# Kernel optimization log

Hardware: AMD Instinct MI355X
Metric: run time of the kernel (lower is better)

Reference implementation:

```python
import jax, jax.numpy as jnp
import numpy as np

CIN = 28
HID1, HID2 = 64, 64
U_IDX, V_IDX = 11, 12
MU_U, SD_U = 0.02, 0.15
MU_V, SD_V = -0.01, 0.12


def setup_inputs() -> dict:
    key = jax.random.key(0)
    ks = jax.random.split(key, 18)
    B, T, H, W = 8, 8, 128, 128
    s = 0.05
    f32 = jnp.float32
    d = {
        "x": jax.random.normal(ks[0], (B, T, CIN, H, W), f32),
        # reduce: Conv2d(Cin, 24, 1)
        "W_red": jax.random.normal(ks[1], (24, CIN), f32) * s,
        "b_red": jnp.zeros((24,), f32),
        # l1: LSTMCell(24, HID1) + Conv2d(HID1, HID1, 1)
        "Wih1": jax.random.normal(ks[2], (4 * HID1, 24), f32) * s,
        "Whh1": jax.random.normal(ks[3], (4 * HID1, HID1), f32) * s,
        "bih1": jnp.zeros((4 * HID1,), f32),
        "bhh1": jnp.zeros((4 * HID1,), f32),
        "Wc1": jax.random.normal(ks[4], (HID1, HID1), f32) * s,
        "bc1": jnp.zeros((HID1,), f32),
        # l2: LSTMCell(HID1, HID2) + Conv2d(HID2, HID2, 1)
        "Wih2": jax.random.normal(ks[5], (4 * HID2, HID1), f32) * s,
        "Whh2": jax.random.normal(ks[6], (4 * HID2, HID2), f32) * s,
        "bih2": jnp.zeros((4 * HID2,), f32),
        "bhh2": jnp.zeros((4 * HID2,), f32),
        "Wc2": jax.random.normal(ks[7], (HID2, HID2), f32) * s,
        "bc2": jnp.zeros((HID2,), f32),
        # head: Conv2d(HID2, 1, 1)
        "W_head": jax.random.normal(ks[8], (1, HID2), f32) * s,
        "b_head": jnp.zeros((1,), f32),
    }
    return d


def _lstm_cell(flat, h, c, Wih, Whh, bih, bhh):
    # PyTorch LSTMCell gate order: i, f, g, o
    g = flat @ Wih.T + bih + h @ Whh.T + bhh
    i, f, gg, o = jnp.split(g, 4, axis=1)
    c = jax.nn.sigmoid(f) * c + jax.nn.sigmoid(i) * jnp.tanh(gg)
    h = jax.nn.sigmoid(o) * jnp.tanh(c)
    return h, c


def _conv1x1(x, W, b):
    # x: [B,C,H,W], W: [O,C]
    return jnp.einsum('bchw,oc->bohw', x, W) + b[None, :, None, None]


def reference(x, W_red, b_red, Wih1, Whh1, bih1, bhh1, Wc1, bc1,
              Wih2, Whh2, bih2, bhh2, Wc2, bc2, W_head, b_head):
    B, T, C, H, W = x.shape
    N = B * H * W
    # de-normalize u/v channels for every timestep (dropout p=0 -> identity)
    x = x.at[:, :, U_IDX].set(x[:, :, U_IDX] * SD_U + MU_U)
    x = x.at[:, :, V_IDX].set(x[:, :, V_IDX] * SD_V + MU_V)

    def step(carry, frame):
        h1, c1, h2, c2 = carry
        inp = _conv1x1(frame, W_red, b_red)                 # [B,24,H,W]
        flat1 = inp.transpose(0, 2, 3, 1).reshape(N, 24)    # pixel-wise rows
        h1, c1 = _lstm_cell(flat1, h1, c1, Wih1, Whh1, bih1, bhh1)
        h1_map = h1.reshape(B, H, W, HID1).transpose(0, 3, 1, 2)
        o1 = _conv1x1(h1_map, Wc1, bc1)                     # [B,HID1,H,W]
        flat2 = o1.transpose(0, 2, 3, 1).reshape(N, HID1)
        h2, c2 = _lstm_cell(flat2, h2, c2, Wih2, Whh2, bih2, bhh2)
        return (h1, c1, h2, c2), None

    z1 = jnp.zeros((N, HID1), x.dtype)
    z2 = jnp.zeros((N, HID2), x.dtype)
    xs = jnp.transpose(x, (1, 0, 2, 3, 4))                  # [T,B,C,H,W]
    (h1, c1, h2, c2), _ = jax.lax.scan(step, (z1, z1, z2, z2), xs)
    # only the last o2 is used by the head
    h2_map = h2.reshape(B, H, W, HID2).transpose(0, 3, 1, 2)
    o2 = _conv1x1(h2_map, Wc2, bc2)                         # [B,HID2,H,W]
    out = _conv1x1(o2, W_head, b_head)                      # [B,1,H,W]
    return out[:, 0]                                        # squeeze(1) -> [B,H,W]
```

## Files before the change

### kernel.cpp

```cpp
#include <hip/hip_runtime.h>

typedef _Float16 f16;
typedef _Float16 f16x4 __attribute__((ext_vector_type(4)));
typedef _Float16 f16x8 __attribute__((ext_vector_type(8)));
typedef float f32x4 __attribute__((ext_vector_type(4)));

#define CIN 28
#define TT 8
#define HW 16384

#define S_SIG  (-1.44269504088896341f)
#define S_TANH ( 2.88539008177792681f)

#define WS_WX    0
#define WS_WHH1  16384
#define WS_W21   49152
#define WS_WHH2  81920
#define WS_BX    114688
#define WS_B2    115712
#define WS_WH    116736
#define WS_BH    116992

__device__ __forceinline__ float lstm_act(float gi, float gf, float gg, float go,
                                          float& c) {
  const float Ei = __builtin_amdgcn_exp2f(gi);
  const float Ef = __builtin_amdgcn_exp2f(gf);
  const float Eg = __builtin_amdgcn_exp2f(gg);
  const float Eo = __builtin_amdgcn_exp2f(go);
  const float pig = (1.f + Ei) * (1.f + Eg);
  const float pf  = 1.f + Ef;
  const float r3  = __builtin_amdgcn_rcpf(pig * pf);
  const float t1  = (Eg - 1.f) * pf;
  const float cn  = r3 * __builtin_fmaf(pig, c, t1);
  c = cn;
  const float Ec  = __builtin_amdgcn_exp2f(cn * S_TANH);
  const float roc = __builtin_amdgcn_rcpf((1.f + Eo) * (1.f + Ec));
  return (Ec - 1.f) * roc;
}

__global__ __launch_bounds__(64) void prep_kernel(
    const float* __restrict__ W_red, const float* __restrict__ b_red,
    const float* __restrict__ Wih1, const float* __restrict__ Whh1,
    const float* __restrict__ bih1, const float* __restrict__ bhh1,
    const float* __restrict__ Wc1,  const float* __restrict__ bc1,
    const float* __restrict__ Wih2, const float* __restrict__ Whh2,
    const float* __restrict__ bih2, const float* __restrict__ bhh2,
    const float* __restrict__ Wc2,  const float* __restrict__ bc2,
    const float* __restrict__ W_head, const float* __restrict__ b_head,
    unsigned char* __restrict__ ws)
{
  const int g = blockIdx.x;
  const int k = threadIdx.x;
  f16* WxH   = (f16*)(ws + WS_WX);
  f16* Whh1H = (f16*)(ws + WS_WHH1);
  f16* W21H  = (f16*)(ws + WS_W21);
  f16* Whh2H = (f16*)(ws + WS_WHH2);
  float* BX  = (float*)(ws + WS_BX);
  float* B2  = (float*)(ws + WS_B2);
  float* WHp = (float*)(ws + WS_WH);
  float* BHp = (float*)(ws + WS_BH);

  const float sc = ((g >> 6) == 2) ? S_TANH : S_SIG;

  float wxv = 0.f;
  if (k < CIN) {
    float s = 0.f;
    for (int r = 0; r < 24; ++r) s += Wih1[g*24 + r] * W_red[r*28 + k];
    wxv = s;
  }
  const float wx11 = __shfl(wxv, 11, 64);
  const float wx12 = __shfl(wxv, 12, 64);
  if (k == 11) wxv *= 0.15f;
  if (k == 12) wxv *= 0.12f;
  if (k < 32) WxH[g*32 + k] = (f16)(wxv * sc);

  Whh1H[g*64 + k] = (f16)(Whh1[g*64 + k] * sc);
  Whh2H[g*64 + k] = (f16)(Whh2[g*64 + k] * sc);

  {
    float s = 0.f;
    for (int m = 0; m < 64; ++m) s += Wih2[g*64 + m] * Wc1[m*64 + k];
    W21H[g*64 + k] = (f16)(s * sc);
  }

  if (k == 0) {
    float bx = bih1[g] + bhh1[g];
    for (int r = 0; r < 24; ++r) bx += Wih1[g*24 + r] * b_red[r];
    bx += wx11 * 0.02f + wx12 * (-0.01f);
    BX[g] = bx * sc;
    float b2v = bih2[g] + bhh2[g];
    for (int m = 0; m < 64; ++m) b2v += Wih2[g*64 + m] * bc1[m];
    B2[g] = b2v * sc;
  }
  if (g == 0) {
    float s = 0.f;
    for (int m = 0; m < 64; ++m) s += W_head[m] * Wc2[m*64 + k];
    WHp[k] = s;
    if (k == 0) {
      float s2 = b_head[0];
      for (int m = 0; m < 64; ++m) s2 += W_head[m] * bc2[m];
      BHp[0] = s2;
    }
  }
}

__global__ __launch_bounds__(256)
__attribute__((amdgpu_waves_per_eu(2, 2)))
void convlstm_main(
    const float* __restrict__ x, const unsigned char* __restrict__ ws,
    float* __restrict__ out)
{
  __shared__ __align__(16) f16 xs[2][64 * 40];
  __shared__ __align__(16) f16 h1buf[2][64 * 72];
  __shared__ __align__(16) f16 h2buf[2][64 * 72];

  const int tid  = threadIdx.x;
  const int lane = tid & 63;
  const int wv   = tid >> 6;
  const int cl   = lane & 15;
  const int qd   = lane >> 4;

  const f16* WxG   = (const f16*)(ws + WS_WX);
  const f16* Whh1G = (const f16*)(ws + WS_WHH1);
  const f16* W21G  = (const f16*)(ws + WS_W21);
  const f16* Whh2G = (const f16*)(ws + WS_WHH2);
  const float* BX  = (const float*)(ws + WS_BX);
  const float* B2  = (const float*)(ws + WS_B2);

  f16x8 wx[4];
  f16x8 whh1k0[4], whh1k1[4];
  f16x8 w21k0[4],  w21k1[4];
  f16x8 whh2k0[4], whh2k1[4];
  f32x4 bxq[4], b2q[4];
#pragma unroll
  for (int P = 0; P < 4; ++P) {
    const int gr = 64*P + 16*wv + cl;
    wx[P]     = *(const f16x8*)(WxG + gr*32 + qd*8);
    whh1k0[P] = *(const f16x8*)(Whh1G + gr*64 + qd*8);
    whh1k1[P] = *(const f16x8*)(Whh1G + gr*64 + 32 + qd*8);
    w21k0[P]  = *(const f16x8*)(W21G  + gr*64 + qd*8);
    w21k1[P]  = *(const f16x8*)(W21G  + gr*64 + 32 + qd*8);
    whh2k0[P] = *(const f16x8*)(Whh2G + gr*64 + qd*8);
    whh2k1[P] = *(const f16x8*)(Whh2G + gr*64 + 32 + qd*8);
    bxq[P] = *(const f32x4*)(BX + 64*P + 16*wv + 4*qd);
    b2q[P] = *(const f32x4*)(B2 + 64*P + 16*wv + 4*qd);
  }

  {
    unsigned* z1 = (unsigned*)&h1buf[0][0];
    unsigned* z2 = (unsigned*)&h2buf[0][0];
#pragma unroll
    for (int i = tid; i < 2304; i += 256) { z1[i] = 0u; z2[i] = 0u; }
  }

  const int gpix = blockIdx.x * 64;
  const float* xb = x + (size_t)(gpix >> 14) * (TT * CIN * HW) + (gpix & (HW - 1));

  const int sp = lane;
  const int cb = wv * 8;

  {
    f16x8 v;
#pragma unroll
    for (int j = 0; j < 8; ++j) {
      const int ch = cb + j;
      v[j] = (ch < CIN) ? (f16)xb[ch*HW + sp] : (f16)0.f;
    }
    *(f16x8*)(&xs[0][sp*40 + cb]) = v;
  }
  __syncthreads();

  float c1s[4][4];
  float c2s[4][4];
#pragma unroll
  for (int a = 0; a < 4; ++a)
#pragma unroll
    for (int b = 0; b < 4; ++b) { c1s[a][b] = 0.f; c2s[a][b] = 0.f; }

#pragma unroll 1
  for (int t = 0; t < TT; ++t) {
    f16x8 xrv;
    if (t + 1 < TT) {
      const float* xt = xb + (size_t)(t + 1) * (CIN * HW);
#pragma unroll
      for (int j = 0; j < 8; ++j) {
        const int ch = cb + j;
        xrv[j] = (ch < CIN) ? (f16)xt[ch*HW + sp] : (f16)0.f;
      }
    }

    const f16* xsr = xs[t & 1];
    const f16* h1r = h1buf[t & 1];
    const f16* h2r = h2buf[t & 1];
    f16* h1w = h1buf[(t + 1) & 1];
    f16* h2w = h2buf[(t + 1) & 1];

#pragma unroll
    for (int mb = 0; mb < 4; ++mb) {
      const int p = 16*mb + cl;
      const f16x8 ax  = *(const f16x8*)(xsr + p*40 + qd*8);
      const f16x8 ah0 = *(const f16x8*)(h1r + p*72 + qd*8);
      const f16x8 ah1 = *(const f16x8*)(h1r + p*72 + 32 + qd*8);
      f32x4 acc[4];
#pragma unroll
      for (int P = 0; P < 4; ++P) {
        acc[P] = __builtin_amdgcn_mfma_f32_16x16x32_f16(whh1k0[P], ah0, bxq[P], 0, 0, 0);
        acc[P] = __builtin_amdgcn_mfma_f32_16x16x32_f16(whh1k1[P], ah1, acc[P], 0, 0, 0);
        acc[P] = __builtin_amdgcn_mfma_f32_16x16x32_f16(wx[P],     ax,  acc[P], 0, 0, 0);
      }
      float hn[4];
#pragma unroll
      for (int r = 0; r < 4; ++r)
        hn[r] = lstm_act(acc[0][r], acc[1][r], acc[2][r], acc[3][r], c1s[mb][r]);
      f16x4 hv; hv[0] = (f16)hn[0]; hv[1] = (f16)hn[1];
      hv[2] = (f16)hn[2]; hv[3] = (f16)hn[3];
      *(f16x4*)(h1w + p*72 + 16*wv + 4*qd) = hv;
    }
    __syncthreads();

    if (t + 1 < TT) {
      f16* xsw = xs[(t + 1) & 1];
      *(f16x8*)(xsw + sp*40 + cb) = xrv;
    }

#pragma unroll
    for (int mb = 0; mb < 4; ++mb) {
      const int p = 16*mb + cl;
      const f16x8 an0 = *(const f16x8*)(h1w + p*72 + qd*8);
      const f16x8 an1 = *(const f16x8*)(h1w + p*72 + 32 + qd*8);
      const f16x8 a20 = *(const f16x8*)(h2r + p*72 + qd*8);
      const f16x8 a21 = *(const f16x8*)(h2r + p*72 + 32 + qd*8);
      f32x4 acc[4];
#pragma unroll
      for (int P = 0; P < 4; ++P) {
        acc[P] = __builtin_amdgcn_mfma_f32_16x16x32_f16(w21k0[P],  an0, b2q[P], 0, 0, 0);
        acc[P] = __builtin_amdgcn_mfma_f32_16x16x32_f16(w21k1[P],  an1, acc[P], 0, 0, 0);
        acc[P] = __builtin_amdgcn_mfma_f32_16x16x32_f16(whh2k0[P], a20, acc[P], 0, 0, 0);
        acc[P] = __builtin_amdgcn_mfma_f32_16x16x32_f16(whh2k1[P], a21, acc[P], 0, 0, 0);
      }
      float hn[4];
#pragma unroll
      for (int r = 0; r < 4; ++r)
        hn[r] = lstm_act(acc[0][r], acc[1][r], acc[2][r], acc[3][r], c2s[mb][r]);
      f16x4 hv; hv[0] = (f16)hn[0]; hv[1] = (f16)hn[1];
      hv[2] = (f16)hn[2]; hv[3] = (f16)hn[3];
      *(f16x4*)(h2w + p*72 + 16*wv + 4*qd) = hv;
    }
    __syncthreads();
  }

  if (tid < 64) {
    const float* wh = (const float*)(ws + WS_WH);
    const f16* row = &h2buf[0][tid * 72];
    float s = *((const float*)(ws + WS_BH));
#pragma unroll
    for (int k = 0; k < 64; ++k) s += (float)row[k] * wh[k];
    out[gpix + tid] = s;
  }
}

extern "C" void kernel_launch(void* const* d_in, const int* in_sizes, int n_in,
                              void* d_out, int out_size, void* d_ws, size_t ws_size,
                              hipStream_t stream) {
  const float* x      = (const float*)d_in[0];
  const float* W_red  = (const float*)d_in[1];
  const float* b_red  = (const float*)d_in[2];
  const float* Wih1   = (const float*)d_in[3];
  const float* Whh1   = (const float*)d_in[4];
  const float* bih1   = (const float*)d_in[5];
  const float* bhh1   = (const float*)d_in[6];
  const float* Wc1    = (const float*)d_in[7];
  const float* bc1    = (const float*)d_in[8];
  const float* Wih2   = (const float*)d_in[9];
  const float* Whh2   = (const float*)d_in[10];
  const float* bih2   = (const float*)d_in[11];
  const float* bhh2   = (const float*)d_in[12];
  const float* Wc2    = (const float*)d_in[13];
  const float* bc2    = (const float*)d_in[14];
  const float* W_head = (const float*)d_in[15];
  const float* b_head = (const float*)d_in[16];

  prep_kernel<<<256, 64, 0, stream>>>(W_red, b_red, Wih1, Whh1, bih1, bhh1,
                                      Wc1, bc1, Wih2, Whh2, bih2, bhh2,
                                      Wc2, bc2, W_head, b_head,
                                      (unsigned char*)d_ws);
  convlstm_main<<<2048, 256, 0, stream>>>(x, (const unsigned char*)d_ws,
                                          (float*)d_out);
}
```

Before: 435.9 us.

## Permute gate rows so each wave owns full gate quads, use 8 waves

The prep kernel now permutes gate weight rows so that the four gates of a hidden unit land in the same MFMA output quad. Each lane then finishes an LSTM cell from one accumulator instead of gathering across four. The main kernel grows from 4 to 8 waves per block, with each wave handling two 16-row tiles instead of four, which halves per-thread weight registers and cell state. The intent is more parallelism and latency hiding per block. The cost is more threads sharing the same LDS and barrier traffic, and smaller x-load vectors per thread.

Measured after the change: 386.2 us. 11.4% less time.

```diff
diff --git a/kernel.cpp b/kernel.cpp
--- a/kernel.cpp
+++ b/kernel.cpp
@@ -1,6 +1,7 @@
 #include <hip/hip_runtime.h>
 
 typedef _Float16 f16;
+typedef _Float16 f16x2 __attribute__((ext_vector_type(2)));
 typedef _Float16 f16x4 __attribute__((ext_vector_type(4)));
 typedef _Float16 f16x8 __attribute__((ext_vector_type(8)));
 typedef float f32x4 __attribute__((ext_vector_type(4)));
@@ -60,7 +61,11 @@
   float* WHp = (float*)(ws + WS_WH);
   float* BHp = (float*)(ws + WS_BH);
 
-  const float sc = ((g >> 6) == 2) ? S_TANH : S_SIG;
+  const int gate = g >> 6;
+  const int col  = g & 63;
+  const int pr = (col >> 3) * 32 + (col & 1) * 16 + ((col >> 1) & 3) * 4 + gate;
+
+  const float sc = (gate == 2) ? S_TANH : S_SIG;
 
   float wxv = 0.f;
   if (k < CIN) {
@@ -72,25 +77,25 @@
   const float wx12 = __shfl(wxv, 12, 64);
   if (k == 11) wxv *= 0.15f;
   if (k == 12) wxv *= 0.12f;
-  if (k < 32) WxH[g*32 + k] = (f16)(wxv * sc);
-
-  Whh1H[g*64 + k] = (f16)(Whh1[g*64 + k] * sc);
-  Whh2H[g*64 + k] = (f16)(Whh2[g*64 + k] * sc);
+  if (k < 32) WxH[pr*32 + k] = (f16)(wxv * sc);
+
+  Whh1H[pr*64 + k] = (f16)(Whh1[g*64 + k] * sc);
+  Whh2H[pr*64 + k] = (f16)(Whh2[g*64 + k] * sc);
 
   {
     float s = 0.f;
     for (int m = 0; m < 64; ++m) s += Wih2[g*64 + m] * Wc1[m*64 + k];
-    W21H[g*64 + k] = (f16)(s * sc);
+    W21H[pr*64 + k] = (f16)(s * sc);
   }
 
   if (k == 0) {
     float bx = bih1[g] + bhh1[g];
     for (int r = 0; r < 24; ++r) bx += Wih1[g*24 + r] * b_red[r];
     bx += wx11 * 0.02f + wx12 * (-0.01f);
-    BX[g] = bx * sc;
+    BX[pr] = bx * sc;
     float b2v = bih2[g] + bhh2[g];
     for (int m = 0; m < 64; ++m) b2v += Wih2[g*64 + m] * bc1[m];
-    B2[g] = b2v * sc;
+    B2[pr] = b2v * sc;
   }
   if (g == 0) {
     float s = 0.f;
@@ -104,8 +109,7 @@
   }
 }
 
-__global__ __launch_bounds__(256)
-__attribute__((amdgpu_waves_per_eu(2, 2)))
+__global__ __launch_bounds__(512, 4)
 void convlstm_main(
     const float* __restrict__ x, const unsigned char* __restrict__ ws,
     float* __restrict__ out)
@@ -127,64 +131,62 @@
   const float* BX  = (const float*)(ws + WS_BX);
   const float* B2  = (const float*)(ws + WS_B2);
 
-  f16x8 wx[4];
-  f16x8 whh1k0[4], whh1k1[4];
-  f16x8 w21k0[4],  w21k1[4];
-  f16x8 whh2k0[4], whh2k1[4];
-  f32x4 bxq[4], b2q[4];
-#pragma unroll
-  for (int P = 0; P < 4; ++P) {
-    const int gr = 64*P + 16*wv + cl;
-    wx[P]     = *(const f16x8*)(WxG + gr*32 + qd*8);
-    whh1k0[P] = *(const f16x8*)(Whh1G + gr*64 + qd*8);
-    whh1k1[P] = *(const f16x8*)(Whh1G + gr*64 + 32 + qd*8);
-    w21k0[P]  = *(const f16x8*)(W21G  + gr*64 + qd*8);
-    w21k1[P]  = *(const f16x8*)(W21G  + gr*64 + 32 + qd*8);
-    whh2k0[P] = *(const f16x8*)(Whh2G + gr*64 + qd*8);
-    whh2k1[P] = *(const f16x8*)(Whh2G + gr*64 + 32 + qd*8);
-    bxq[P] = *(const f32x4*)(BX + 64*P + 16*wv + 4*qd);
-    b2q[P] = *(const f32x4*)(B2 + 64*P + 16*wv + 4*qd);
+  f16x8 wx[2];
+  f16x8 whh1[2][2], w21[2][2], whh2[2][2];
+  f32x4 bxq[2], b2q[2];
+#pragma unroll
+  for (int rt = 0; rt < 2; ++rt) {
+    const int pr = wv*32 + rt*16 + cl;
+    wx[rt]      = *(const f16x8*)(WxG + pr*32 + qd*8);
+    whh1[rt][0] = *(const f16x8*)(Whh1G + pr*64 + qd*8);
+    whh1[rt][1] = *(const f16x8*)(Whh1G + pr*64 + 32 + qd*8);
+    w21[rt][0]  = *(const f16x8*)(W21G  + pr*64 + qd*8);
+    w21[rt][1]  = *(const f16x8*)(W21G  + pr*64 + 32 + qd*8);
+    whh2[rt][0] = *(const f16x8*)(Whh2G + pr*64 + qd*8);
+    whh2[rt][1] = *(const f16x8*)(Whh2G + pr*64 + 32 + qd*8);
+    bxq[rt] = *(const f32x4*)(BX + wv*32 + rt*16 + 4*qd);
+    b2q[rt] = *(const f32x4*)(B2 + wv*32 + rt*16 + 4*qd);
   }
 
   {
     unsigned* z1 = (unsigned*)&h1buf[0][0];
     unsigned* z2 = (unsigned*)&h2buf[0][0];
 #pragma unroll
-    for (int i = tid; i < 2304; i += 256) { z1[i] = 0u; z2[i] = 0u; }
+    for (int i = tid; i < 2304; i += 512) { z1[i] = 0u; z2[i] = 0u; }
   }
 
   const int gpix = blockIdx.x * 64;
   const float* xb = x + (size_t)(gpix >> 14) * (TT * CIN * HW) + (gpix & (HW - 1));
 
   const int sp = lane;
-  const int cb = wv * 8;
+  const int cg = wv;
 
   {
-    f16x8 v;
-#pragma unroll
-    for (int j = 0; j < 8; ++j) {
-      const int ch = cb + j;
+    f16x4 v;
+#pragma unroll
+    for (int j = 0; j < 4; ++j) {
+      const int ch = cg*4 + j;
       v[j] = (ch < CIN) ? (f16)xb[ch*HW + sp] : (f16)0.f;
     }
-    *(f16x8*)(&xs[0][sp*40 + cb]) = v;
+    *(f16x4*)(&xs[0][sp*40 + cg*4]) = v;
   }
   __syncthreads();
 
-  float c1s[4][4];
-  float c2s[4][4];
+  float c1s[4][2];
+  float c2s[4][2];
 #pragma unroll
   for (int a = 0; a < 4; ++a)
 #pragma unroll
-    for (int b = 0; b < 4; ++b) { c1s[a][b] = 0.f; c2s[a][b] = 0.f; }
+    for (int b = 0; b < 2; ++b) { c1s[a][b] = 0.f; c2s[a][b] = 0.f; }
 
 #pragma unroll 1
   for (int t = 0; t < TT; ++t) {
-    f16x8 xrv;
+    f16x4 xrv;
     if (t + 1 < TT) {
       const float* xt = xb + (size_t)(t + 1) * (CIN * HW);
 #pragma unroll
-      for (int j = 0; j < 8; ++j) {
-        const int ch = cb + j;
+      for (int j = 0; j < 4; ++j) {
+        const int ch = cg*4 + j;
         xrv[j] = (ch < CIN) ? (f16)xt[ch*HW + sp] : (f16)0.f;
       }
     }
@@ -201,26 +203,23 @@
       const f16x8 ax  = *(const f16x8*)(xsr + p*40 + qd*8);
       const f16x8 ah0 = *(const f16x8*)(h1r + p*72 + qd*8);
       const f16x8 ah1 = *(const f16x8*)(h1r + p*72 + 32 + qd*8);
-      f32x4 acc[4];
-#pragma unroll
-      for (int P = 0; P < 4; ++P) {
-        acc[P] = __builtin_amdgcn_mfma_f32_16x16x32_f16(whh1k0[P], ah0, bxq[P], 0, 0, 0);
-        acc[P] = __builtin_amdgcn_mfma_f32_16x16x32_f16(whh1k1[P], ah1, acc[P], 0, 0, 0);
-        acc[P] = __builtin_amdgcn_mfma_f32_16x16x32_f16(wx[P],     ax,  acc[P], 0, 0, 0);
+      float hn[2];
+#pragma unroll
+      for (int rt = 0; rt < 2; ++rt) {
+        f32x4 acc;
+        acc = __builtin_amdgcn_mfma_f32_16x16x32_f16(whh1[rt][0], ah0, bxq[rt], 0, 0, 0);
+        acc = __builtin_amdgcn_mfma_f32_16x16x32_f16(whh1[rt][1], ah1, acc, 0, 0, 0);
+        acc = __builtin_amdgcn_mfma_f32_16x16x32_f16(wx[rt],      ax,  acc, 0, 0, 0);
+        hn[rt] = lstm_act(acc[0], acc[1], acc[2], acc[3], c1s[mb][rt]);
       }
-      float hn[4];
-#pragma unroll
-      for (int r = 0; r < 4; ++r)
-        hn[r] = lstm_act(acc[0][r], acc[1][r], acc[2][r], acc[3][r], c1s[mb][r]);
-      f16x4 hv; hv[0] = (f16)hn[0]; hv[1] = (f16)hn[1];
-      hv[2] = (f16)hn[2]; hv[3] = (f16)hn[3];
-      *(f16x4*)(h1w + p*72 + 16*wv + 4*qd) = hv;
+      f16x2 hv; hv[0] = (f16)hn[0]; hv[1] = (f16)hn[1];
+      *(f16x2*)(h1w + p*72 + 8*wv + 2*qd) = hv;
     }
     __syncthreads();
 
     if (t + 1 < TT) {
       f16* xsw = xs[(t + 1) & 1];
-      *(f16x8*)(xsw + sp*40 + cb) = xrv;
+      *(f16x4*)(xsw + sp*40 + cg*4) = xrv;
     }
 
 #pragma unroll
@@ -230,21 +229,18 @@
       const f16x8 an1 = *(const f16x8*)(h1w + p*72 + 32 + qd*8);
       const f16x8 a20 = *(const f16x8*)(h2r + p*72 + qd*8);
       const f16x8 a21 = *(const f16x8*)(h2r + p*72 + 32 + qd*8);
-      f32x4 acc[4];
-#pragma unroll
-      for (int P = 0; P < 4; ++P) {
-        acc[P] = __builtin_amdgcn_mfma_f32_16x16x32_f16(w21k0[P],  an0, b2q[P], 0, 0, 0);
-        acc[P] = __builtin_amdgcn_mfma_f32_16x16x32_f16(w21k1[P],  an1, acc[P], 0, 0, 0);
-        acc[P] = __builtin_amdgcn_mfma_f32_16x16x32_f16(whh2k0[P], a20, acc[P], 0, 0, 0);
-        acc[P] = __builtin_amdgcn_mfma_f32_16x16x32_f16(whh2k1[P], a21, acc[P], 0, 0, 0);
+      float hn[2];
+#pragma unroll
+      for (int rt = 0; rt < 2; ++rt) {
+        f32x4 acc;
+        acc = __builtin_amdgcn_mfma_f32_16x16x32_f16(w21[rt][0],  an0, b2q[rt], 0, 0, 0);
+        acc = __builtin_amdgcn_mfma_f32_16x16x32_f16(w21[rt][1],  an1, acc, 0, 0, 0);
+        acc = __builtin_amdgcn_mfma_f32_16x16x32_f16(whh2[rt][0], a20, acc, 0, 0, 0);
+        acc = __builtin_amdgcn_mfma_f32_16x16x32_f16(whh2[rt][1], a21, acc, 0, 0, 0);
+        hn[rt] = lstm_act(acc[0], acc[1], acc[2], acc[3], c2s[mb][rt]);
       }
-      float hn[4];
-#pragma unroll
-      for (int r = 0; r < 4; ++r)
-        hn[r] = lstm_act(acc[0][r], acc[1][r], acc[2][r], acc[3][r], c2s[mb][r]);
-      f16x4 hv; hv[0] = (f16)hn[0]; hv[1] = (f16)hn[1];
-      hv[2] = (f16)hn[2]; hv[3] = (f16)hn[3];
-      *(f16x4*)(h2w + p*72 + 16*wv + 4*qd) = hv;
+      f16x2 hv; hv[0] = (f16)hn[0]; hv[1] = (f16)hn[1];
+      *(f16x2*)(h2w + p*72 + 8*wv + 2*qd) = hv;
     }
     __syncthreads();
   }
@@ -284,6 +280,6 @@
                                       Wc1, bc1, Wih2, Whh2, bih2, bhh2,
                                       Wc2, bc2, W_head, b_head,
                                       (unsigned char*)d_ws);
-  convlstm_main<<<2048, 256, 0, stream>>>(x, (const unsigned char*)d_ws,
+  convlstm_main<<<2048, 512, 0, stream>>>(x, (const unsigned char*)d_ws,
                                           (float*)d_out);
 }
```
